# Performance work log

Hardware: AMD Instinct MI355X
Metric: run time of the kernel (lower is better)

Reference implementation:

```python
import jax, jax.numpy as jnp
import numpy as np

N = 200000   # nodes
R = 4        # relations
E = 1000000  # edges per relation
B = 1024     # graphs in batch


def _graph_conv(h, s, d, ew, W, b):
    """DGL GraphConv, norm='both', optional edge_weight. h:[N,F_in] -> [N,F_out]."""
    n = h.shape[0]
    ones = jnp.ones(s.shape[0], dtype=h.dtype)
    out_deg = jnp.clip(jax.ops.segment_sum(ones, s, num_segments=n), 1.0)
    in_deg = jnp.clip(jax.ops.segment_sum(ones, d, num_segments=n), 1.0)
    hs = h * jax.lax.rsqrt(out_deg)[:, None]          # src-side norm
    m = hs[s]                                         # gather: [E, F_in]
    if ew is not None:
        m = m * ew[:, None]
    agg = jax.ops.segment_sum(m, d, num_segments=n)   # scatter-sum: [N, F_in]
    rst = agg * jax.lax.rsqrt(in_deg)[:, None]        # dst-side norm
    return rst @ W + b


def _hetero_layer(h, src, dst, ew, W, b):
    out = None
    for r in range(R):
        ewr = None if ew is None else ew[r]
        o = _graph_conv(h, src[r], dst[r], ewr, W[r], b[r])
        out = o if out is None else out + o
    return out


def setup_inputs() -> dict:
    key = jax.random.key(0)
    ks = jax.random.split(key, 10)
    feat = jax.random.normal(ks[0], (N, 2), dtype=jnp.float32)
    src = jax.random.randint(ks[1], (R, E), 0, N, dtype=jnp.int32)
    dst = jax.random.randint(ks[2], (R, E), 0, N, dtype=jnp.int32)
    ew = jax.random.uniform(ks[3], (R, E), dtype=jnp.float32)
    graph_ids = jnp.sort(jax.random.randint(ks[4], (N,), 0, B, dtype=jnp.int32))
    W1 = jax.random.normal(ks[5], (R, 2, 16), dtype=jnp.float32) * 0.5
    b1 = jnp.zeros((R, 16), dtype=jnp.float32)
    W2 = jax.random.normal(ks[6], (R, 16, 16), dtype=jnp.float32) * 0.25
    b2 = jnp.zeros((R, 16), dtype=jnp.float32)
    Wc = jax.random.normal(ks[7], (16, 2), dtype=jnp.float32) * 0.25
    bc = jnp.zeros((2,), dtype=jnp.float32)
    return {"feat": feat, "src": src, "dst": dst, "ew": ew,
            "graph_ids": graph_ids, "W1": W1, "b1": b1,
            "W2": W2, "b2": b2, "Wc": Wc, "bc": bc}


def reference(feat, src, dst, ew, graph_ids, W1, b1, W2, b2, Wc, bc):
    # layer 1: per-relation weighted GraphConv, summed over relations
    h = _hetero_layer(feat, src, dst, ew, W1, b1)
    h = jax.nn.relu(h)
    # layer 2: no edge weights (kwargs not forwarded in original code)
    h = _hetero_layer(h, src, dst, None, W2, b2)
    # mean_nodes per graph in the batch
    sums = jax.ops.segment_sum(h, graph_ids, num_segments=B)          # [B,16]
    cnts = jax.ops.segment_sum(jnp.ones((N,), h.dtype), graph_ids, num_segments=B)
    hg = sums / jnp.clip(cnts, 1.0)[:, None]
    return hg @ Wc + bc                                               # [B,2]
```

## Files before the change

kernel.cpp:

```cpp
#include <hip/hip_runtime.h>
#include <hip/hip_fp16.h>

#define NN 200000
#define RR 4
#define EE 1000000
#define BB 1024
#define RN (RR*NN)

#define BSH 7
#define BSZ 128
#define NB 1563
#define RK (RR*NB)
#define EPB 8192
#define SBT 1024
#define BPR ((EE + EPB - 1) / EPB)
#define GSLOTS 32
#define CAPB 1024

#define SRC_OF(u)  (((u) >> 7) & 0x3FFFF)
#define DL_OF(u)   ((int)((u) & 127))
#define DEG_OF(u)  ((u) >> 25)

#define OFF_POOL   0
#define OFF_CNT    (OFF_POOL + BB*16)
#define OFF_GCUR_S (OFF_CNT + BB)
#define OFF_GCUR_D (OFF_GCUR_S + RK)
#define ZERO_UNITS (OFF_GCUR_D + RK)
#define OFF_DEGB   ZERO_UNITS
#define OFF_INVI   (OFF_DEGB + RN/4)
#define OFF_RW16   (OFF_INVI + RN)
#define OFF_AGG1   (OFF_RW16 + RN/2)
#define OFF_H1H    (OFF_AGG1 + RN*2)
#define OFF_KW_    (OFF_H1H + NN*8)
#define OFF_KW     (OFF_KW_ + (OFF_KW_ & 1))


__global__ __launch_bounds__(SBT) void k_scat(const int* __restrict__ src,
                                              const int* __restrict__ dst,
                                              const float* __restrict__ ew,
                                              int* __restrict__ gcur_s,
                                              int* __restrict__ gcur_d,
                                              unsigned char* __restrict__ srcbin,
                                              long long* __restrict__ kw) {
  __shared__ int cntS[NB];
  __shared__ int baseS[NB];
  __shared__ int lcurS[NB];
  __shared__ int cntD[NB];
  __shared__ int baseD[NB];
  __shared__ int lcurD[NB];
  int t = threadIdx.x, r = blockIdx.y, c0 = blockIdx.x * EPB;
  for (int i = t; i < NB; i += SBT) { cntS[i] = 0; cntD[i] = 0; }
  __syncthreads();
  for (int i = t; i < EPB; i += SBT) {
    int e = c0 + i;
    if (e < EE) {
      atomicAdd(&cntS[src[r * EE + e] >> BSH], 1);
      atomicAdd(&cntD[dst[r * EE + e] >> BSH], 1);
    }
  }
  __syncthreads();
  for (int b = t; b < NB; b += SBT) {
    int v = cntS[b];
    baseS[b] = v ? atomicAdd(&gcur_s[r * NB + b], v) : 0;
    lcurS[b] = 0;
    int w = cntD[b];
    baseD[b] = w ? atomicAdd(&gcur_d[r * NB + b], w) : 0;
    lcurD[b] = 0;
  }
  __syncthreads();
  for (int i = t; i < EPB; i += SBT) {
    int e = c0 + i;
    if (e < EE) {
      int idx = r * EE + e;
      int s = src[idx], d = dst[idx];
      int bs = s >> BSH;
      int offs = baseS[bs] + atomicAdd(&lcurS[bs], 1);
      if (offs < CAPB)
        srcbin[(size_t)(r * NB + bs) * CAPB + offs] = (unsigned char)(s & (BSZ - 1));
      int bd = d >> BSH;
      int offd = baseD[bd] + atomicAdd(&lcurD[bd], 1);
      if (offd < CAPB) {
        unsigned short ewh = __half_as_ushort(__float2half_rn(ew[idx]));
        unsigned low = (unsigned)(d & (BSZ - 1)) | ((unsigned)s << 7);
        kw[(size_t)(r * NB + bd) * CAPB + offd] =
            (long long)(((unsigned long long)ewh << 32) | low);
      }
    }
  }
}

__global__ __launch_bounds__(128) void k_deg(const unsigned char* __restrict__ srcbin,
                                             const int* __restrict__ gcur_s,
                                             unsigned char* __restrict__ degb) {
  __shared__ int cnt[BSZ];
  int t = threadIdx.x, b = blockIdx.x, r = blockIdx.y;
  cnt[t] = 0;
  __syncthreads();
  int k = r * NB + b;
  size_t st = (size_t)k * CAPB;
  int m = min(gcur_s[k], CAPB);
  for (int e = t; e < m; e += 128) atomicAdd(&cnt[srcbin[st + e]], 1);
  __syncthreads();
  int n = (b << BSH) + t;
  if (n < NN) degb[r * NN + n] = (unsigned char)min(max(cnt[t], 1), 63);
}

__global__ __launch_bounds__(256) void k_l1a(long long* __restrict__ kw,
                                             const int* __restrict__ gcur_d,
                                             const unsigned char* __restrict__ degb,
                                             const float* __restrict__ feat,
                                             float* __restrict__ invi,
                                             unsigned short* __restrict__ rw16,
                                             float* __restrict__ agg1) {
  __shared__ long long bufraw[CAPB];
  __shared__ long long bufsort[CAPB];
  __shared__ int cnt[BSZ];
  __shared__ int scn[BSZ];
  __shared__ int cur[BSZ];
  __shared__ float la[BSZ * 3];
  int t = threadIdx.x, b = blockIdx.x, r = blockIdx.y;
  int n0 = b << BSH;
  int k = r * NB + b;
  size_t st = (size_t)k * CAPB;
  int m = min(gcur_d[k], CAPB);
  if (t < BSZ) { cnt[t] = 0; la[t * 3] = 0.f; la[t * 3 + 1] = 0.f; }
  for (int i = t; i < m; i += 256) bufraw[i] = kw[st + i];
  __syncthreads();
  for (int i = t; i < m; i += 256)
    atomicAdd(&cnt[DL_OF((unsigned)bufraw[i])], 1);
  __syncthreads();
  if (t < BSZ) scn[t] = cnt[t];
  __syncthreads();
  for (int off = 1; off < BSZ; off <<= 1) {
    int v = (t < BSZ && t >= off) ? scn[t - off] : 0;
    __syncthreads();
    if (t < BSZ) scn[t] += v;
    __syncthreads();
  }
  if (t < BSZ) {
    int excl = scn[t] - cnt[t];
    cur[t] = excl;
    int n = n0 + t;
    if (n < NN) {
      invi[r * NN + n] = rsqrtf((float)max(cnt[t], 1));
      rw16[r * NN + n] = (unsigned short)excl;
    }
  }
  __syncthreads();
  for (int i = t; i < m; i += 256) {
    long long kv = bufraw[i];
    unsigned low = (unsigned)kv;
    int s = SRC_OF(low);
    unsigned dg = degb[r * NN + s];
    float ewf = __half2float(__ushort_as_half((unsigned short)((unsigned long long)kv >> 32)));
    unsigned short w1h = __half_as_ushort(__float2half_rn(ewf * rsqrtf((float)dg)));
    bufraw[i] = (long long)(((unsigned long long)w1h << 32) |
                            (unsigned long long)(low | (dg << 25)));
  }
  __syncthreads();
  for (int i = t; i < m; i += 256) {
    long long kv = bufraw[i];
    bufsort[atomicAdd(&cur[DL_OF((unsigned)kv)], 1)] = kv;
  }
  __syncthreads();
  {
    unsigned* up = (unsigned*)kw + 2 * st + CAPB;
    for (int i = t; i < m; i += 256) up[i] = (unsigned)bufsort[i];
  }
  {
    int f = t & 1, grp = t >> 1;
    int seg = (m + BSZ - 1) >> 7;
    int e = grp * seg;
    int e1 = min(e + seg, m);
    float acc = 0.f;
    int dlprev = -1, dlfirst = -1;
    for (; e < e1; e++) {
      long long kv = bufsort[e];
      unsigned low = (unsigned)kv;
      int dl = DL_OF(low);
      int s = SRC_OF(low);
      float w = __half2float(__ushort_as_half((unsigned short)((unsigned long long)kv >> 32)));
      float fv = feat[s * 2 + f];
      if (dl != dlprev) {
        if (dlprev < 0) dlfirst = dl;
        else if (dlprev == dlfirst) atomicAdd(&la[dlprev * 3 + f], acc);
        else la[dlprev * 3 + f] = acc;
        acc = 0.f; dlprev = dl;
      }
      acc += fv * w;
    }
    if (dlprev >= 0) atomicAdd(&la[dlprev * 3 + f], acc);
  }
  __syncthreads();
  if (t < BSZ) {
    int n = n0 + t;
    if (n < NN)
      ((float2*)agg1)[r * NN + n] = make_float2(la[t * 3], la[t * 3 + 1]);
  }
}

__device__ __forceinline__ unsigned pack2h(float a, float b) {
  __half2 h = __floats2half2_rn(a, b);
  return *reinterpret_cast<unsigned*>(&h);
}

__global__ __launch_bounds__(256) void k_l1b(const float* __restrict__ agg1,
                                             const float* __restrict__ invi,
                                             const float* __restrict__ W1,
                                             const float* __restrict__ b1,
                                             __half* __restrict__ h1h) {
  __shared__ float sW[RR * 2 * 16];
  __shared__ float sb[16];
  int t = threadIdx.x, b = blockIdx.x;
  if (t < RR * 2 * 16) sW[t] = W1[t];
  if (t < 16) {
    float s = 0.f;
    for (int r = 0; r < RR; r++) s += b1[r * 16 + t];
    sb[t] = s;
  }
  __syncthreads();
  int n = b * 256 + t;
  if (n >= NN) return;
  float acc[16];
#pragma unroll
  for (int j = 0; j < 16; j++) acc[j] = sb[j];
#pragma unroll
  for (int r = 0; r < RR; r++) {
    float iv = invi[r * NN + n];
    float2 a = ((const float2*)agg1)[r * NN + n];
    float a0 = a.x * iv, a1 = a.y * iv;
#pragma unroll
    for (int j = 0; j < 16; j++)
      acc[j] += a0 * sW[(r * 2 + 0) * 16 + j] + a1 * sW[(r * 2 + 1) * 16 + j];
  }
#pragma unroll
  for (int j = 0; j < 16; j++) acc[j] = fmaxf(acc[j], 0.f);
  uint4 u0, u1;
  u0.x = pack2h(acc[0], acc[1]);  u0.y = pack2h(acc[2], acc[3]);
  u0.z = pack2h(acc[4], acc[5]);  u0.w = pack2h(acc[6], acc[7]);
  u1.x = pack2h(acc[8], acc[9]);  u1.y = pack2h(acc[10], acc[11]);
  u1.z = pack2h(acc[12], acc[13]); u1.w = pack2h(acc[14], acc[15]);
  uint4* o = (uint4*)(h1h + (size_t)n * 16);
  o[0] = u0; o[1] = u1;
}

__device__ __forceinline__ void acc8(float* acc, uint4 u, float w) {
  float2 p;
  p = __half22float2(*(__half2*)&u.x); acc[0] += p.x * w; acc[1] += p.y * w;
  p = __half22float2(*(__half2*)&u.y); acc[2] += p.x * w; acc[3] += p.y * w;
  p = __half22float2(*(__half2*)&u.z); acc[4] += p.x * w; acc[5] += p.y * w;
  p = __half22float2(*(__half2*)&u.w); acc[6] += p.x * w; acc[7] += p.y * w;
}

__global__ __launch_bounds__(256) void k_l2(const long long* __restrict__ kw,
                                            const int* __restrict__ gcur_d,
                                            const unsigned short* __restrict__ rw16,
                                            const __half* __restrict__ h1h,
                                            const float* __restrict__ invi,
                                            const float* __restrict__ W2,
                                            const int* __restrict__ gid,
                                            float* __restrict__ pool,
                                            float* __restrict__ cnt) {
  __shared__ float agg[BSZ * 17];
  __shared__ float sW[16 * 16];
  __shared__ int   sg[BSZ];
  __shared__ unsigned short srw[BSZ + 1];
  __shared__ float gslot[GSLOTS * 16];
  __shared__ int   cslot[GSLOTS];
  __shared__ int   present[GSLOTS];
  int t = threadIdx.x, b = blockIdx.x, r = blockIdx.y;
  int n0 = b << BSH;
  int k = r * NB + b;
  int m = min(gcur_d[k], CAPB);
  sW[t] = W2[r * 256 + t];
  if (t < GSLOTS) { cslot[t] = 0; present[t] = 0; }
  for (int i = t; i < GSLOTS * 16; i += 256) gslot[i] = 0.f;
  if (t < BSZ) {
    int n = n0 + t;
    srw[t] = (n < NN) ? rw16[r * NN + n] : (unsigned short)m;
  }
  if (t == BSZ) srw[BSZ] = (unsigned short)m;
  __syncthreads();
  const uint4* h4p = (const uint4*)h1h;
  const unsigned* rb = (const unsigned*)kw + 2 * (size_t)k * CAPB + CAPB;
  int f8 = t & 1, g = t >> 1;
  int e = srw[g], en = srw[g + 1];
  float acc[8];
#pragma unroll
  for (int j = 0; j < 8; j++) acc[j] = 0.f;
  for (; e + 3 < en; e += 4) {
    unsigned r0 = rb[e], r1 = rb[e + 1], r2 = rb[e + 2], r3 = rb[e + 3];
    uint4 u0 = h4p[(size_t)SRC_OF(r0) * 2 + f8];
    uint4 u1 = h4p[(size_t)SRC_OF(r1) * 2 + f8];
    uint4 u2 = h4p[(size_t)SRC_OF(r2) * 2 + f8];
    uint4 u3 = h4p[(size_t)SRC_OF(r3) * 2 + f8];
    acc8(acc, u0, rsqrtf((float)DEG_OF(r0)));
    acc8(acc, u1, rsqrtf((float)DEG_OF(r1)));
    acc8(acc, u2, rsqrtf((float)DEG_OF(r2)));
    acc8(acc, u3, rsqrtf((float)DEG_OF(r3)));
  }
  for (; e < en; e++) {
    unsigned rr = rb[e];
    uint4 u = h4p[(size_t)SRC_OF(rr) * 2 + f8];
    acc8(acc, u, rsqrtf((float)DEG_OF(rr)));
  }
#pragma unroll
  for (int j = 0; j < 8; j++) agg[g * 17 + 8 * f8 + j] = acc[j];
  __syncthreads();
  int n = n0 + t;
  int g0 = gid[n0];
  bool valid = (t < BSZ) && (n < NN);
  float out[16];
#pragma unroll
  for (int j = 0; j < 16; j++) out[j] = 0.f;
  if (valid) {
    float iv = invi[r * NN + n];
#pragma unroll
    for (int kk = 0; kk < 16; kk++) {
      float a = agg[t * 17 + kk] * iv;
#pragma unroll
      for (int j = 0; j < 16; j++) out[j] += a * sW[kk * 16 + j];
    }
  }
  __syncthreads();
  if (t < BSZ) {
    sg[t] = valid ? (gid[n] - g0) : -1;
#pragma unroll
    for (int j = 0; j < 16; j++) agg[t * 17 + j] = out[j];
  }
  __syncthreads();
  {
    int f = t & 15, i0 = t >> 4;
    for (int i = i0; i < BSZ; i += 16) {
      int gsN = sg[i];
      if (gsN < 0) continue;
      float v = agg[i * 17 + f];
      if (gsN < GSLOTS) {
        atomicAdd(&gslot[gsN * 16 + f], v);
        if (f == 0) {
          present[gsN] = 1;
          if (r == 0) atomicAdd(&cslot[gsN], 1);
        }
      } else {
        atomicAdd(&pool[(g0 + gsN) * 16 + f], v);
        if (f == 0 && r == 0) atomicAdd(&cnt[g0 + gsN], 1.0f);
      }
    }
  }
  __syncthreads();
  if (t < GSLOTS * 16) {
    int gsN = t >> 4, f = t & 15;
    if (present[gsN]) atomicAdd(&pool[(g0 + gsN) * 16 + f], gslot[t]);
  }
  if (r == 0 && t < GSLOTS && cslot[t] > 0)
    atomicAdd(&cnt[g0 + t], (float)cslot[t]);
}

__global__ __launch_bounds__(256) void k_final(const float* __restrict__ pool,
                                               const float* __restrict__ cnt,
                                               const float* __restrict__ b2,
                                               const float* __restrict__ Wc,
                                               const float* __restrict__ bc,
                                               float* __restrict__ out) {
  int b = blockIdx.x * 256 + threadIdx.x;
  if (b >= BB) return;
  float c = cnt[b];
  float inv = 1.0f / fmaxf(c, 1.0f);
  float o0 = bc[0], o1 = bc[1];
#pragma unroll
  for (int j = 0; j < 16; j++) {
    float sb = 0.f;
    for (int r = 0; r < RR; r++) sb += b2[r * 16 + j];
    float v = (pool[b * 16 + j] + c * sb) * inv;
    o0 += v * Wc[j * 2 + 0];
    o1 += v * Wc[j * 2 + 1];
  }
  out[b * 2 + 0] = o0;
  out[b * 2 + 1] = o1;
}

extern "C" void kernel_launch(void* const* d_in, const int* in_sizes, int n_in,
                              void* d_out, int out_size, void* d_ws, size_t ws_size,
                              hipStream_t stream) {
  const float* feat = (const float*)d_in[0];
  const int*   src  = (const int*)d_in[1];
  const int*   dst  = (const int*)d_in[2];
  const float* ew   = (const float*)d_in[3];
  const int*   gid  = (const int*)d_in[4];
  const float* W1   = (const float*)d_in[5];
  const float* b1   = (const float*)d_in[6];
  const float* W2   = (const float*)d_in[7];
  const float* b2   = (const float*)d_in[8];
  const float* Wc   = (const float*)d_in[9];
  const float* bc   = (const float*)d_in[10];

  char* ws = (char*)d_ws;
  float* pool   = (float*)(ws + (size_t)OFF_POOL   * 4);
  float* cnt    = (float*)(ws + (size_t)OFF_CNT    * 4);
  int*   gcur_s = (int*)  (ws + (size_t)OFF_GCUR_S * 4);
  int*   gcur_d = (int*)  (ws + (size_t)OFF_GCUR_D * 4);
  unsigned char*  degb = (unsigned char*) (ws + (size_t)OFF_DEGB * 4);
  float* invi   = (float*)(ws + (size_t)OFF_INVI   * 4);
  unsigned short* rw16 = (unsigned short*)(ws + (size_t)OFF_RW16 * 4);
  float* agg1   = (float*)(ws + (size_t)OFF_AGG1   * 4);
  unsigned char* srcbin = (unsigned char*)(ws + (size_t)OFF_AGG1 * 4);
  __half* h1h   = (__half*)(ws + (size_t)OFF_H1H   * 4);
  long long* kw = (long long*)(ws + (size_t)OFF_KW * 4);

  hipMemsetAsync(d_ws, 0, (size_t)ZERO_UNITS * 4, stream);

  k_scat  <<<dim3(BPR, RR), SBT, 0, stream>>>(src, dst, ew, gcur_s, gcur_d, srcbin, kw);
  k_deg   <<<dim3(NB, RR), 128, 0, stream>>>(srcbin, gcur_s, degb);
  k_l1a   <<<dim3(NB, RR), 256, 0, stream>>>(kw, gcur_d, degb, feat, invi, rw16, agg1);
  k_l1b   <<<(NN + 255) / 256, 256, 0, stream>>>(agg1, invi, W1, b1, h1h);
  k_l2    <<<dim3(NB, RR), 256, 0, stream>>>(kw, gcur_d, rw16, h1h, invi, W2, gid, pool, cnt);
  k_final <<<(BB + 255) / 256, 256, 0, stream>>>(pool, cnt, b2, Wc, bc, (float*)d_out);
}
```

Baseline: 345.2 us.

## Replace fine-grained edge binning with two-level coarse/fine partition and sort

```diff
diff --git a/kernel.cpp b/kernel.cpp
--- a/kernel.cpp
+++ b/kernel.cpp
@@ -11,6 +11,10 @@
 #define BSZ 128
 #define NB 1563
 #define RK (RR*NB)
+#define CSH 12
+#define CNODES 4096
+#define CC 49
+#define CAPC 22528
 #define EPB 8192
 #define SBT 1024
 #define BPR ((EE + EPB - 1) / EPB)
@@ -23,49 +27,42 @@
 
 #define OFF_POOL   0
 #define OFF_CNT    (OFF_POOL + BB*16)
-#define OFF_GCUR_S (OFF_CNT + BB)
-#define OFF_GCUR_D (OFF_GCUR_S + RK)
-#define ZERO_UNITS (OFF_GCUR_D + RK)
+#define OFF_GCS    (OFF_CNT + BB)
+#define OFF_GCD    (OFF_GCS + RR*CC)
+#define OFF_GFIN   (OFF_GCD + RR*CC)
+#define ZERO_UNITS (OFF_GFIN + RK)
 #define OFF_DEGB   ZERO_UNITS
 #define OFF_INVI   (OFF_DEGB + RN/4)
 #define OFF_RW16   (OFF_INVI + RN)
 #define OFF_AGG1   (OFF_RW16 + RN/2)
+#define OFF_SBC    OFF_AGG1
 #define OFF_H1H    (OFF_AGG1 + RN*2)
-#define OFF_KW_    (OFF_H1H + NN*8)
-#define OFF_KW     (OFF_KW_ + (OFF_KW_ & 1))
-
-
-__global__ __launch_bounds__(SBT) void k_scat(const int* __restrict__ src,
+#define OFF_KWC    (OFF_H1H + NN*8)
+#define OFF_KW4    (OFF_KWC + RR*CC*CAPC)
+
+
+__global__ __launch_bounds__(SBT) void k_part(const int* __restrict__ src,
                                               const int* __restrict__ dst,
-                                              const float* __restrict__ ew,
-                                              int* __restrict__ gcur_s,
-                                              int* __restrict__ gcur_d,
-                                              unsigned char* __restrict__ srcbin,
-                                              long long* __restrict__ kw) {
-  __shared__ int cntS[NB];
-  __shared__ int baseS[NB];
-  __shared__ int lcurS[NB];
-  __shared__ int cntD[NB];
-  __shared__ int baseD[NB];
-  __shared__ int lcurD[NB];
+                                              int* __restrict__ gcs,
+                                              int* __restrict__ gcd,
+                                              unsigned short* __restrict__ sbc,
+                                              unsigned* __restrict__ kwc) {
+  __shared__ int cS[CC], bS[CC], lS[CC];
+  __shared__ int cD[CC], bD[CC], lD[CC];
   int t = threadIdx.x, r = blockIdx.y, c0 = blockIdx.x * EPB;
-  for (int i = t; i < NB; i += SBT) { cntS[i] = 0; cntD[i] = 0; }
+  if (t < CC) { cS[t] = 0; cD[t] = 0; }
   __syncthreads();
   for (int i = t; i < EPB; i += SBT) {
     int e = c0 + i;
     if (e < EE) {
-      atomicAdd(&cntS[src[r * EE + e] >> BSH], 1);
-      atomicAdd(&cntD[dst[r * EE + e] >> BSH], 1);
+      atomicAdd(&cS[src[r * EE + e] >> CSH], 1);
+      atomicAdd(&cD[dst[r * EE + e] >> CSH], 1);
     }
   }
   __syncthreads();
-  for (int b = t; b < NB; b += SBT) {
-    int v = cntS[b];
-    baseS[b] = v ? atomicAdd(&gcur_s[r * NB + b], v) : 0;
-    lcurS[b] = 0;
-    int w = cntD[b];
-    baseD[b] = w ? atomicAdd(&gcur_d[r * NB + b], w) : 0;
-    lcurD[b] = 0;
+  if (t < CC) {
+    int v = cS[t]; bS[t] = v ? atomicAdd(&gcs[r * CC + t], v) : 0; lS[t] = 0;
+    int w = cD[t]; bD[t] = w ? atomicAdd(&gcd[r * CC + t], w) : 0; lD[t] = 0;
   }
   __syncthreads();
   for (int i = t; i < EPB; i += SBT) {
@@ -73,100 +70,124 @@
     if (e < EE) {
       int idx = r * EE + e;
       int s = src[idx], d = dst[idx];
-      int bs = s >> BSH;
-      int offs = baseS[bs] + atomicAdd(&lcurS[bs], 1);
-      if (offs < CAPB)
-        srcbin[(size_t)(r * NB + bs) * CAPB + offs] = (unsigned char)(s & (BSZ - 1));
-      int bd = d >> BSH;
-      int offd = baseD[bd] + atomicAdd(&lcurD[bd], 1);
-      if (offd < CAPB) {
-        unsigned short ewh = __half_as_ushort(__float2half_rn(ew[idx]));
-        unsigned low = (unsigned)(d & (BSZ - 1)) | ((unsigned)s << 7);
-        kw[(size_t)(r * NB + bd) * CAPB + offd] =
-            (long long)(((unsigned long long)ewh << 32) | low);
-      }
+      int cs = s >> CSH;
+      int offs = bS[cs] + atomicAdd(&lS[cs], 1);
+      if (offs < CAPC)
+        sbc[(size_t)(r * CC + cs) * CAPC + offs] = (unsigned short)(s & (CNODES - 1));
+      int cd = d >> CSH;
+      int offd = bD[cd] + atomicAdd(&lD[cd], 1);
+      if (offd < CAPC)
+        kwc[(size_t)(r * CC + cd) * CAPC + offd] =
+            ((unsigned)(d & (CNODES - 1)) << 20) | (unsigned)e;
     }
   }
 }
 
-__global__ __launch_bounds__(128) void k_deg(const unsigned char* __restrict__ srcbin,
-                                             const int* __restrict__ gcur_s,
-                                             unsigned char* __restrict__ degb) {
-  __shared__ int cnt[BSZ];
-  int t = threadIdx.x, b = blockIdx.x, r = blockIdx.y;
-  cnt[t] = 0;
-  __syncthreads();
-  int k = r * NB + b;
-  size_t st = (size_t)k * CAPB;
-  int m = min(gcur_s[k], CAPB);
-  for (int e = t; e < m; e += 128) atomicAdd(&cnt[srcbin[st + e]], 1);
-  __syncthreads();
-  int n = (b << BSH) + t;
-  if (n < NN) degb[r * NN + n] = (unsigned char)min(max(cnt[t], 1), 63);
-}
-
-__global__ __launch_bounds__(256) void k_l1a(long long* __restrict__ kw,
-                                             const int* __restrict__ gcur_d,
+__global__ __launch_bounds__(1024) void k_fine(const unsigned* __restrict__ kwc,
+                                               const unsigned short* __restrict__ sbc,
+                                               const int* __restrict__ gcs,
+                                               const int* __restrict__ gcd,
+                                               unsigned* __restrict__ kw4,
+                                               int* __restrict__ gfin,
+                                               float* __restrict__ invi,
+                                               unsigned short* __restrict__ rw16,
+                                               unsigned char* __restrict__ degb) {
+  __shared__ int h[CNODES];
+  __shared__ int s4[1024];
+  __shared__ int sfb[33];
+  int t = threadIdx.x, c = blockIdx.x, r = blockIdx.y;
+  int kc = r * CC + c;
+  size_t stc = (size_t)kc * CAPC;
+  int nrec = min(gcd[kc], CAPC);
+  for (int i = t; i < CNODES; i += 1024) h[i] = 0;
+  __syncthreads();
+  for (int i = t; i < nrec; i += 1024) atomicAdd(&h[kwc[stc + i] >> 20], 1);
+  __syncthreads();
+  int a0 = h[4 * t], a1 = h[4 * t + 1], a2 = h[4 * t + 2], a3 = h[4 * t + 3];
+  int tot = a0 + a1 + a2 + a3;
+  s4[t] = tot;
+  __syncthreads();
+  for (int off = 1; off < 1024; off <<= 1) {
+    int v = (t >= off) ? s4[t - off] : 0;
+    __syncthreads();
+    s4[t] += v;
+    __syncthreads();
+  }
+  int base = s4[t] - tot;
+  if ((t & 31) == 0) sfb[(4 * t) >> 7] = base;
+  if (t == 1023) sfb[32] = s4[1023];
+  __syncthreads();
+  int n0 = c * CNODES;
+  int e0 = base, e1 = base + a0, e2 = e1 + a1, e3 = e2 + a2;
+  {
+    int cl = 4 * t;
+    int sb = sfb[cl >> 7];
+    int n = n0 + cl;
+    if (n < NN)     { invi[r*NN+n]   = rsqrtf((float)max(a0,1)); rw16[r*NN+n]   = (unsigned short)min(e0-sb, CAPB); }
+    if (n + 1 < NN) { invi[r*NN+n+1] = rsqrtf((float)max(a1,1)); rw16[r*NN+n+1] = (unsigned short)min(e1-sb, CAPB); }
+    if (n + 2 < NN) { invi[r*NN+n+2] = rsqrtf((float)max(a2,1)); rw16[r*NN+n+2] = (unsigned short)min(e2-sb, CAPB); }
+    if (n + 3 < NN) { invi[r*NN+n+3] = rsqrtf((float)max(a3,1)); rw16[r*NN+n+3] = (unsigned short)min(e3-sb, CAPB); }
+  }
+  if (t < 32) {
+    int kb = c * 32 + t;
+    if (kb < NB) gfin[r * NB + kb] = min(sfb[t + 1] - sfb[t], CAPB);
+  }
+  __syncthreads();
+  h[4 * t] = e0; h[4 * t + 1] = e1; h[4 * t + 2] = e2; h[4 * t + 3] = e3;
+  __syncthreads();
+  for (int i = t; i < nrec; i += 1024) {
+    unsigned rc = kwc[stc + i];
+    int cl = rc >> 20;
+    int pos = atomicAdd(&h[cl], 1);
+    int fb = cl >> 7;
+    int fpos = pos - sfb[fb];
+    if (fpos < CAPB)
+      kw4[(size_t)(r * NB + c * 32 + fb) * CAPB + fpos] =
+          (unsigned)(cl & 127) | ((rc & 0xFFFFFu) << 7);
+  }
+  __syncthreads();
+  for (int i = t; i < CNODES; i += 1024) h[i] = 0;
+  __syncthreads();
+  int nsrc = min(gcs[kc], CAPC);
+  for (int i = t; i < nsrc; i += 1024) atomicAdd(&h[sbc[stc + i]], 1);
+  __syncthreads();
+  for (int i = t; i < CNODES; i += 1024) {
+    int n = n0 + i;
+    if (n < NN) degb[r * NN + n] = (unsigned char)min(max(h[i], 1), 63);
+  }
+}
+
+__global__ __launch_bounds__(256) void k_l1a(unsigned* __restrict__ kw4,
+                                             const int* __restrict__ gfin,
+                                             const int* __restrict__ src,
+                                             const float* __restrict__ ew,
                                              const unsigned char* __restrict__ degb,
                                              const float* __restrict__ feat,
-                                             float* __restrict__ invi,
-                                             unsigned short* __restrict__ rw16,
                                              float* __restrict__ agg1) {
-  __shared__ long long bufraw[CAPB];
-  __shared__ long long bufsort[CAPB];
-  __shared__ int cnt[BSZ];
-  __shared__ int scn[BSZ];
-  __shared__ int cur[BSZ];
+  __shared__ unsigned buf4[CAPB];
+  __shared__ long long buf8[CAPB];
   __shared__ float la[BSZ * 3];
   int t = threadIdx.x, b = blockIdx.x, r = blockIdx.y;
   int n0 = b << BSH;
   int k = r * NB + b;
   size_t st = (size_t)k * CAPB;
-  int m = min(gcur_d[k], CAPB);
-  if (t < BSZ) { cnt[t] = 0; la[t * 3] = 0.f; la[t * 3 + 1] = 0.f; }
-  for (int i = t; i < m; i += 256) bufraw[i] = kw[st + i];
-  __syncthreads();
-  for (int i = t; i < m; i += 256)
-    atomicAdd(&cnt[DL_OF((unsigned)bufraw[i])], 1);
-  __syncthreads();
-  if (t < BSZ) scn[t] = cnt[t];
-  __syncthreads();
-  for (int off = 1; off < BSZ; off <<= 1) {
-    int v = (t < BSZ && t >= off) ? scn[t - off] : 0;
-    __syncthreads();
-    if (t < BSZ) scn[t] += v;
-    __syncthreads();
-  }
-  if (t < BSZ) {
-    int excl = scn[t] - cnt[t];
-    cur[t] = excl;
-    int n = n0 + t;
-    if (n < NN) {
-      invi[r * NN + n] = rsqrtf((float)max(cnt[t], 1));
-      rw16[r * NN + n] = (unsigned short)excl;
-    }
-  }
+  int m = gfin[k];
+  if (t < BSZ) { la[t * 3] = 0.f; la[t * 3 + 1] = 0.f; }
+  for (int i = t; i < m; i += 256) buf4[i] = kw4[st + i];
   __syncthreads();
   for (int i = t; i < m; i += 256) {
-    long long kv = bufraw[i];
-    unsigned low = (unsigned)kv;
-    int s = SRC_OF(low);
+    unsigned rc = buf4[i];
+    int dl = rc & 127;
+    int eid = (rc >> 7) & 0xFFFFF;
+    int s = src[r * EE + eid];
+    float ewf = ew[r * EE + eid];
     unsigned dg = degb[r * NN + s];
-    float ewf = __half2float(__ushort_as_half((unsigned short)((unsigned long long)kv >> 32)));
     unsigned short w1h = __half_as_ushort(__float2half_rn(ewf * rsqrtf((float)dg)));
-    bufraw[i] = (long long)(((unsigned long long)w1h << 32) |
-                            (unsigned long long)(low | (dg << 25)));
-  }
-  __syncthreads();
-  for (int i = t; i < m; i += 256) {
-    long long kv = bufraw[i];
-    bufsort[atomicAdd(&cur[DL_OF((unsigned)kv)], 1)] = kv;
-  }
-  __syncthreads();
-  {
-    unsigned* up = (unsigned*)kw + 2 * st + CAPB;
-    for (int i = t; i < m; i += 256) up[i] = (unsigned)bufsort[i];
-  }
+    unsigned low = (unsigned)dl | ((unsigned)s << 7) | (dg << 25);
+    buf8[i] = (long long)(((unsigned long long)w1h << 32) | low);
+    kw4[st + i] = low;
+  }
+  __syncthreads();
   {
     int f = t & 1, grp = t >> 1;
     int seg = (m + BSZ - 1) >> 7;
@@ -175,7 +196,7 @@
     float acc = 0.f;
     int dlprev = -1, dlfirst = -1;
     for (; e < e1; e++) {
-      long long kv = bufsort[e];
+      long long kv = buf8[e];
       unsigned low = (unsigned)kv;
       int dl = DL_OF(low);
       int s = SRC_OF(low);
@@ -252,8 +273,8 @@
   p = __half22float2(*(__half2*)&u.w); acc[6] += p.x * w; acc[7] += p.y * w;
 }
 
-__global__ __launch_bounds__(256) void k_l2(const long long* __restrict__ kw,
-                                            const int* __restrict__ gcur_d,
+__global__ __launch_bounds__(256) void k_l2(const unsigned* __restrict__ kw4,
+                                            const int* __restrict__ gfin,
                                             const unsigned short* __restrict__ rw16,
                                             const __half* __restrict__ h1h,
                                             const float* __restrict__ invi,
@@ -271,7 +292,7 @@
   int t = threadIdx.x, b = blockIdx.x, r = blockIdx.y;
   int n0 = b << BSH;
   int k = r * NB + b;
-  int m = min(gcur_d[k], CAPB);
+  int m = min(gfin[k], CAPB);
   sW[t] = W2[r * 256 + t];
   if (t < GSLOTS) { cslot[t] = 0; present[t] = 0; }
   for (int i = t; i < GSLOTS * 16; i += 256) gslot[i] = 0.f;
@@ -282,7 +303,7 @@
   if (t == BSZ) srw[BSZ] = (unsigned short)m;
   __syncthreads();
   const uint4* h4p = (const uint4*)h1h;
-  const unsigned* rb = (const unsigned*)kw + 2 * (size_t)k * CAPB + CAPB;
+  const unsigned* rb = kw4 + (size_t)k * CAPB;
   int f8 = t & 1, g = t >> 1;
   int e = srw[g], en = srw[g + 1];
   float acc[8];
@@ -395,24 +416,26 @@
   const float* bc   = (const float*)d_in[10];
 
   char* ws = (char*)d_ws;
-  float* pool   = (float*)(ws + (size_t)OFF_POOL   * 4);
-  float* cnt    = (float*)(ws + (size_t)OFF_CNT    * 4);
-  int*   gcur_s = (int*)  (ws + (size_t)OFF_GCUR_S * 4);
-  int*   gcur_d = (int*)  (ws + (size_t)OFF_GCUR_D * 4);
+  float* pool   = (float*)(ws + (size_t)OFF_POOL * 4);
+  float* cnt    = (float*)(ws + (size_t)OFF_CNT  * 4);
+  int*   gcs    = (int*)  (ws + (size_t)OFF_GCS  * 4);
+  int*   gcd    = (int*)  (ws + (size_t)OFF_GCD  * 4);
+  int*   gfin   = (int*)  (ws + (size_t)OFF_GFIN * 4);
   unsigned char*  degb = (unsigned char*) (ws + (size_t)OFF_DEGB * 4);
-  float* invi   = (float*)(ws + (size_t)OFF_INVI   * 4);
+  float* invi   = (float*)(ws + (size_t)OFF_INVI * 4);
   unsigned short* rw16 = (unsigned short*)(ws + (size_t)OFF_RW16 * 4);
-  float* agg1   = (float*)(ws + (size_t)OFF_AGG1   * 4);
-  unsigned char* srcbin = (unsigned char*)(ws + (size_t)OFF_AGG1 * 4);
-  __half* h1h   = (__half*)(ws + (size_t)OFF_H1H   * 4);
-  long long* kw = (long long*)(ws + (size_t)OFF_KW * 4);
+  float* agg1   = (float*)(ws + (size_t)OFF_AGG1 * 4);
+  unsigned short* sbc  = (unsigned short*)(ws + (size_t)OFF_SBC * 4);
+  __half* h1h   = (__half*)(ws + (size_t)OFF_H1H * 4);
+  unsigned* kwc = (unsigned*)(ws + (size_t)OFF_KWC * 4);
+  unsigned* kw4 = (unsigned*)(ws + (size_t)OFF_KW4 * 4);
 
   hipMemsetAsync(d_ws, 0, (size_t)ZERO_UNITS * 4, stream);
 
-  k_scat  <<<dim3(BPR, RR), SBT, 0, stream>>>(src, dst, ew, gcur_s, gcur_d, srcbin, kw);
-  k_deg   <<<dim3(NB, RR), 128, 0, stream>>>(srcbin, gcur_s, degb);
-  k_l1a   <<<dim3(NB, RR), 256, 0, stream>>>(kw, gcur_d, degb, feat, invi, rw16, agg1);
+  k_part  <<<dim3(BPR, RR), SBT, 0, stream>>>(src, dst, gcs, gcd, sbc, kwc);
+  k_fine  <<<dim3(CC, RR), 1024, 0, stream>>>(kwc, sbc, gcs, gcd, kw4, gfin, invi, rw16, degb);
+  k_l1a   <<<dim3(NB, RR), 256, 0, stream>>>(kw4, gfin, src, ew, degb, feat, agg1);
   k_l1b   <<<(NN + 255) / 256, 256, 0, stream>>>(agg1, invi, W1, b1, h1h);
-  k_l2    <<<dim3(NB, RR), 256, 0, stream>>>(kw, gcur_d, rw16, h1h, invi, W2, gid, pool, cnt);
+  k_l2    <<<dim3(NB, RR), 256, 0, stream>>>(kw4, gfin, rw16, h1h, invi, W2, gid, pool, cnt);
   k_final <<<(BB + 255) / 256, 256, 0, stream>>>(pool, cnt, b2, Wc, bc, (float*)d_out);
 }
```

Measured after the change: 411.1 us. +19.1%, slower.
